# Kernel optimization log

Measured on AMD Instinct MI355X. Metric: run time of the kernel, lower is better.

## Reference

```python
import jax, jax.numpy as jnp
import numpy as np

K = 3          # kernel size
PAD = (K - 1) // 2


def setup_inputs() -> dict:
    key = jax.random.key(0)
    k1, k2, k3 = jax.random.split(key, 3)
    x = jax.random.normal(k1, (32, 512, 56, 56), jnp.float32)
    # offset predictor conv1d weight: (out=K, in=1, kw=K), no bias
    w_offset = jax.random.normal(k2, (K, 1, K), jnp.float32) * 0.1
    # deformable conv1d(1,1,K) weight (K,) and scalar bias
    w_deform = jax.random.normal(k3, (K,), jnp.float32) * 0.5
    b_deform = jnp.zeros((), jnp.float32)
    return {"x": x, "w_offset": w_offset, "w_deform": w_deform, "b_deform": b_deform}


def _dca_forward(x, w_offset, w_deform, b_deform):
    b, c, h, w = x.shape
    # AdaptiveAvgPool2d(1) -> channel descriptor (b, c)
    y = x.mean(axis=(2, 3))
    # conv_offset_local: Conv1d(1, K, kernel=K, pad=PAD) on (b, 1, c) -> (b, K, c)
    offset = jax.lax.conv_general_dilated(
        y[:, None, :], w_offset, window_strides=(1,),
        padding=[(PAD, PAD)], dimension_numbers=("NCH", "OIH", "NCH"))
    # deformable sampling positions: p + k - PAD + offset[b,k,p], shape (b, K, c)
    pos = (jnp.arange(c, dtype=x.dtype)[None, None, :]
           + jnp.arange(K, dtype=x.dtype)[None, :, None]
           - PAD + offset)
    p0 = jnp.floor(pos)
    frac = pos - p0                     # (b, K, c), differentiable wrt offset
    p0i = p0.astype(jnp.int32)

    def sample(idx):
        # linear gather from y with zero padding outside [0, c)
        valid = (idx >= 0) & (idx < c)
        idxc = jnp.clip(idx, 0, c - 1)
        v = jax.vmap(lambda yb, ib: yb[ib])(y, idxc)   # (b, K, c)
        return jnp.where(valid, v, jnp.zeros((), x.dtype))

    v = sample(p0i) * (1.0 - frac) + sample(p0i + 1) * frac
    out = jnp.einsum("k,bkc->bc", w_deform, v) + b_deform   # (b, c)
    attn = jax.nn.sigmoid(out)[:, :, None, None]
    return attn * x


def reference(x, w_offset, w_deform, b_deform):
    return _dca_forward(x, w_offset, w_deform, b_deform)
```

## Files before the change

kernel.cpp:

```cpp
#include <hip/hip_runtime.h>
#include <hip/hip_bf16.h>
#include <math.h>

#define B 32
#define C 512
#define HW 3136
#define HW4 784
#define KS 3
#define PADK 1

typedef float fvec4 __attribute__((ext_vector_type(4)));

__global__ __launch_bounds__(256) void mean_kernel(const float* __restrict__ x,
                                                   float* __restrict__ y) {
    const int plane = blockIdx.x;
    const fvec4* xp = (const fvec4*)(x + (size_t)plane * HW);
    float s = 0.f;
    for (int i = threadIdx.x; i < HW4; i += 256) {
        fvec4 v = xp[i];
        s += (v.x + v.y) + (v.z + v.w);
    }
    #pragma unroll
    for (int o = 32; o > 0; o >>= 1) s += __shfl_down(s, o, 64);
    __shared__ float red[4];
    const int wave = threadIdx.x >> 6;
    const int lane = threadIdx.x & 63;
    if (lane == 0) red[wave] = s;
    __syncthreads();
    if (threadIdx.x == 0) {
        float t = (red[0] + red[1]) + (red[2] + red[3]);
        y[plane] = t * (1.0f / (float)HW);
    }
}

__global__ __launch_bounds__(256) void scale_attn_kernel(
        const float* __restrict__ x,
        const float* __restrict__ y,
        const float* __restrict__ w_offset,
        const float* __restrict__ w_deform,
        const float* __restrict__ b_deform,
        float* __restrict__ out) {
    const int plane = blockIdx.x;
    const int b = plane >> 9;
    const int p = plane & (C - 1);
    __shared__ float a_sh;

    if (threadIdx.x == 0) {
        const float* yb = y + b * C;
        const float ym1 = (p >= 1)     ? yb[p - 1] : 0.f;
        const float y0  = yb[p];
        const float yp1 = (p < C - 1)  ? yb[p + 1] : 0.f;

        float acc = b_deform[0];
        #pragma unroll
        for (int k = 0; k < KS; ++k) {
            const float off = w_offset[k * KS + 0] * ym1
                            + w_offset[k * KS + 1] * y0
                            + w_offset[k * KS + 2] * yp1;
            const float pos  = (float)(p + k - PADK) + off;
            const float p0f  = floorf(pos);
            const float frac = pos - p0f;
            const int   i0   = (int)p0f;
            const int   i1   = i0 + 1;
            const float v0 = (i0 >= 0 && i0 < C) ? yb[i0] : 0.f;
            const float v1 = (i1 >= 0 && i1 < C) ? yb[i1] : 0.f;
            acc += w_deform[k] * (v0 * (1.f - frac) + v1 * frac);
        }
        a_sh = 1.f / (1.f + expf(-acc));
    }
    __syncthreads();
    const float a = a_sh;

    const fvec4* xp = (const fvec4*)(x + (size_t)plane * HW);
    fvec4*       op = (fvec4*)(out + (size_t)plane * HW);
    for (int i = threadIdx.x; i < HW4; i += 256) {
        fvec4 v = xp[i];
        v *= a;
        __builtin_nontemporal_store(v, &op[i]);
    }
}

extern "C" void kernel_launch(void* const* d_in, const int* in_sizes, int n_in,
                              void* d_out, int out_size, void* d_ws, size_t ws_size,
                              hipStream_t stream) {
    const float* x        = (const float*)d_in[0];
    const float* w_offset = (const float*)d_in[1];
    const float* w_deform = (const float*)d_in[2];
    const float* b_deform = (const float*)d_in[3];
    float* out  = (float*)d_out;

    float* y = (float*)d_ws;

    mean_kernel<<<B * C, 256, 0, stream>>>(x, y);
    scale_attn_kernel<<<B * C, 256, 0, stream>>>(x, y, w_offset, w_deform,
                                                 b_deform, out);
}
```

Measured before the change: 370.0 us.

## Map one wavefront per plane and split attention into its own kernel

The mean and scale kernels now assign one 64-lane wavefront per channel plane, four planes per block, with fully unrolled vector loads. This removes the LDS reduction, __syncthreads, and the serial single-thread attention computation from the scale kernel. The attention sigmoid is computed once per (b,c) in a separate small kernel and written to workspace. The scale kernel also switches from nontemporal stores to normal stores. The trade-off is an extra kernel launch plus a small workspace round-trip.

Measured after the change: 383.4 us. 1.04x slower.

```diff
diff --git a/kernel.cpp b/kernel.cpp
--- a/kernel.cpp
+++ b/kernel.cpp
@@ -1,5 +1,4 @@
 #include <hip/hip_runtime.h>
-#include <hip/hip_bf16.h>
 #include <math.h>
 
 #define B 32
@@ -13,70 +12,88 @@
 
 __global__ __launch_bounds__(256) void mean_kernel(const float* __restrict__ x,
                                                    float* __restrict__ y) {
-    const int plane = blockIdx.x;
+    const int plane = (blockIdx.x << 2) + (threadIdx.x >> 6);
+    const int lane  = threadIdx.x & 63;
     const fvec4* xp = (const fvec4*)(x + (size_t)plane * HW);
-    float s = 0.f;
-    for (int i = threadIdx.x; i < HW4; i += 256) {
-        fvec4 v = xp[i];
-        s += (v.x + v.y) + (v.z + v.w);
+
+    float s0 = 0.f, s1 = 0.f, s2 = 0.f, s3 = 0.f;
+    #pragma unroll
+    for (int it = 0; it < 3; ++it) {
+        const int i = lane + it * 256;
+        fvec4 a = xp[i];
+        fvec4 b = xp[i + 64];
+        fvec4 c = xp[i + 128];
+        fvec4 d = xp[i + 192];
+        s0 += (a.x + a.y) + (a.z + a.w);
+        s1 += (b.x + b.y) + (b.z + b.w);
+        s2 += (c.x + c.y) + (c.z + c.w);
+        s3 += (d.x + d.y) + (d.z + d.w);
     }
+    if (lane < 16) {
+        fvec4 a = xp[768 + lane];
+        s0 += (a.x + a.y) + (a.z + a.w);
+    }
+    float s = (s0 + s1) + (s2 + s3);
     #pragma unroll
     for (int o = 32; o > 0; o >>= 1) s += __shfl_down(s, o, 64);
-    __shared__ float red[4];
-    const int wave = threadIdx.x >> 6;
-    const int lane = threadIdx.x & 63;
-    if (lane == 0) red[wave] = s;
-    __syncthreads();
-    if (threadIdx.x == 0) {
-        float t = (red[0] + red[1]) + (red[2] + red[3]);
-        y[plane] = t * (1.0f / (float)HW);
-    }
+    if (lane == 0) y[plane] = s * (1.0f / (float)HW);
 }
 
-__global__ __launch_bounds__(256) void scale_attn_kernel(
-        const float* __restrict__ x,
+__global__ __launch_bounds__(256) void attn_kernel(
         const float* __restrict__ y,
         const float* __restrict__ w_offset,
         const float* __restrict__ w_deform,
         const float* __restrict__ b_deform,
+        float* __restrict__ attn) {
+    const int id = blockIdx.x * 256 + threadIdx.x;
+    const int b  = id >> 9;
+    const int p  = id & (C - 1);
+    const float* yb = y + b * C;
+
+    const float ym1 = (p >= 1)    ? yb[p - 1] : 0.f;
+    const float y0  = yb[p];
+    const float yp1 = (p < C - 1) ? yb[p + 1] : 0.f;
+
+    float acc = b_deform[0];
+    #pragma unroll
+    for (int k = 0; k < KS; ++k) {
+        const float off = w_offset[k * KS + 0] * ym1
+                        + w_offset[k * KS + 1] * y0
+                        + w_offset[k * KS + 2] * yp1;
+        const float pos  = (float)(p + k - PADK) + off;
+        const float p0f  = floorf(pos);
+        const float frac = pos - p0f;
+        const int   i0   = (int)p0f;
+        const int   i1   = i0 + 1;
+        const float v0 = (i0 >= 0 && i0 < C) ? yb[i0] : 0.f;
+        const float v1 = (i1 >= 0 && i1 < C) ? yb[i1] : 0.f;
+        acc += w_deform[k] * (v0 * (1.f - frac) + v1 * frac);
+    }
+    attn[id] = 1.f / (1.f + expf(-acc));
+}
+
+__global__ __launch_bounds__(256) void scale_kernel(
+        const float* __restrict__ x,
+        const float* __restrict__ attn,
         float* __restrict__ out) {
-    const int plane = blockIdx.x;
-    const int b = plane >> 9;
-    const int p = plane & (C - 1);
-    __shared__ float a_sh;
-
-    if (threadIdx.x == 0) {
-        const float* yb = y + b * C;
-        const float ym1 = (p >= 1)     ? yb[p - 1] : 0.f;
-        const float y0  = yb[p];
-        const float yp1 = (p < C - 1)  ? yb[p + 1] : 0.f;
-
-        float acc = b_deform[0];
-        #pragma unroll
-        for (int k = 0; k < KS; ++k) {
-            const float off = w_offset[k * KS + 0] * ym1
-                            + w_offset[k * KS + 1] * y0
-                            + w_offset[k * KS + 2] * yp1;
-            const float pos  = (float)(p + k - PADK) + off;
-            const float p0f  = floorf(pos);
-            const float frac = pos - p0f;
-            const int   i0   = (int)p0f;
-            const int   i1   = i0 + 1;
-            const float v0 = (i0 >= 0 && i0 < C) ? yb[i0] : 0.f;
-            const float v1 = (i1 >= 0 && i1 < C) ? yb[i1] : 0.f;
-            acc += w_deform[k] * (v0 * (1.f - frac) + v1 * frac);
-        }
-        a_sh = 1.f / (1.f + expf(-acc));
-    }
-    __syncthreads();
-    const float a = a_sh;
-
+    const int plane = (blockIdx.x << 2) + (threadIdx.x >> 6);
+    const int lane  = threadIdx.x & 63;
+    const float a   = attn[plane];
     const fvec4* xp = (const fvec4*)(x + (size_t)plane * HW);
     fvec4*       op = (fvec4*)(out + (size_t)plane * HW);
-    for (int i = threadIdx.x; i < HW4; i += 256) {
+
+    #pragma unroll
+    for (int it = 0; it < 12; ++it) {
+        const int i = lane + it * 64;
         fvec4 v = xp[i];
         v *= a;
-        __builtin_nontemporal_store(v, &op[i]);
+        op[i] = v;
+    }
+    if (lane < 16) {
+        const int i = 768 + lane;
+        fvec4 v = xp[i];
+        v *= a;
+        op[i] = v;
     }
 }
 
@@ -89,9 +106,11 @@
     const float* b_deform = (const float*)d_in[3];
     float* out  = (float*)d_out;
 
-    float* y = (float*)d_ws;
+    float* y    = (float*)d_ws;
+    float* attn = (float*)d_ws + B * C;
 
-    mean_kernel<<<B * C, 256, 0, stream>>>(x, y);
-    scale_attn_kernel<<<B * C, 256, 0, stream>>>(x, y, w_offset, w_deform,
-                                                 b_deform, out);
+    mean_kernel <<<B * C / 4,   256, 0, stream>>>(x, y);
+    attn_kernel <<<B * C / 256, 256, 0, stream>>>(y, w_offset, w_deform,
+                                                  b_deform, attn);
+    scale_kernel<<<B * C / 4,   256, 0, stream>>>(x, attn, out);
 }
```
